# Performance work log

Measured on AMD Instinct MI355X. Metric: run time of the kernel, lower is better.

The kernel has to match this reference:

```python
import jax, jax.numpy as jnp
import numpy as np

N = 150_000      # nodes
E = 4_800_000    # edges (avg degree 32)
F_IN = 3
H = 16           # hidden_dim (module default)
DEPTH = 2        # -> DEPTH-1 = 1 mid layer


def setup_inputs() -> dict:
    key = jax.random.key(0)
    ks = jax.random.split(key, 6)
    x = jax.random.normal(ks[0], (N, F_IN), dtype=jnp.float32)
    edge_index = jax.random.randint(ks[1], (2, E), 0, N, dtype=jnp.int64)
    W_in = jax.random.normal(ks[2], (F_IN, H), dtype=jnp.float32) / np.sqrt(F_IN)
    b_in = jnp.zeros((H,), jnp.float32)
    W_mid = jax.random.normal(ks[3], (DEPTH - 1, H, H), dtype=jnp.float32) / np.sqrt(H)
    b_mid = jnp.zeros((DEPTH - 1, H), jnp.float32)
    W_out = jax.random.normal(ks[4], (H, 1), dtype=jnp.float32) / np.sqrt(H)
    b_out = jnp.zeros((1,), jnp.float32)
    return dict(x=x, edge_index=edge_index, W_in=W_in, b_in=b_in,
                W_mid=W_mid, b_mid=b_mid, W_out=W_out, b_out=b_out)


def _gcn(x, src, dst, norm, W, b):
    # GCNConv: X' = D^{-1/2}(A+I)D^{-1/2} X W + b  (self loops already in src/dst)
    h = x @ W                                   # [N, out]
    msg = h[src] * norm[:, None]                # gather + scale, [E+N, out]
    agg = jax.ops.segment_sum(msg, dst, num_segments=N)  # scatter-add
    return agg + b


def reference(x, edge_index, W_in, b_in, W_mid, b_mid, W_out, b_out):
    loops = jnp.arange(N, dtype=edge_index.dtype)
    src = jnp.concatenate([edge_index[0], loops])
    dst = jnp.concatenate([edge_index[1], loops])
    deg = jax.ops.segment_sum(jnp.ones_like(dst, x.dtype), dst, num_segments=N)
    dinv = jax.lax.rsqrt(jnp.where(deg > 0, deg, 1.0))  # deg >= 1 due to self loops
    norm = dinv[src] * dinv[dst]                # symmetric normalization per edge

    h = jax.nn.relu(_gcn(x, src, dst, norm, W_in, b_in))
    for i in range(DEPTH - 1):                  # dropout p=0.0 -> identity
        h = jax.nn.relu(_gcn(h, src, dst, norm, W_mid[i], b_mid[i]))
    out = _gcn(h, src, dst, norm, W_out, b_out)
    return jax.nn.sigmoid(out)                  # [N, 1]
```

## Files before the change

### kernel.cpp

```cpp
#include <hip/hip_runtime.h>
#include <math.h>

#define NN 150000
#define NE 4800000
#define HD 16
#define NBUCK 586
#define BSH 8
#define NBLK 256
#define CHUNK 18750
#define HCH 9375
#define NSCAN 150016
#define SCANB 147

__device__ __forceinline__ float bf2f(unsigned short u) {
    return __uint_as_float(((unsigned int)u) << 16);
}
__device__ __forceinline__ unsigned short f2bf(float f) {
    unsigned int x = __float_as_uint(f);
    return (unsigned short)((x + 0x7FFFu + ((x >> 16) & 1u)) >> 16);
}


__global__ __launch_bounds__(512) void k_part_count(const int* __restrict__ dst,
                                                    int* __restrict__ C) {
    __shared__ int h[NBUCK];
    for (int i = threadIdx.x; i < NBUCK; i += 512) h[i] = 0;
    __syncthreads();
    int base = blockIdx.x * CHUNK;
    for (int i = threadIdx.x; i < CHUNK; i += 512)
        atomicAdd(&h[dst[base + i] >> BSH], 1);
    __syncthreads();
    for (int i = threadIdx.x; i < NBUCK; i += 512) C[i * NBLK + blockIdx.x] = h[i];
}

__global__ void k_scanA(int* __restrict__ C, int* __restrict__ psum) {
    __shared__ int s[1024];
    int t = threadIdx.x;
    int i = blockIdx.x * 1024 + t;
    int v = (i < NSCAN) ? C[i] : 0;
    s[t] = v;
    __syncthreads();
    for (int off = 1; off < 1024; off <<= 1) {
        int x = (t >= off) ? s[t - off] : 0;
        __syncthreads();
        s[t] += x;
        __syncthreads();
    }
    if (i < NSCAN) C[i] = s[t] - v;
    if (t == 1023) psum[blockIdx.x] = s[1023];
}

__global__ void k_scanB(int* __restrict__ psum) {
    __shared__ int s[512];
    int t = threadIdx.x;
    int v = (t < SCANB) ? psum[t] : 0;
    s[t] = v;
    __syncthreads();
    for (int off = 1; off < 512; off <<= 1) {
        int x = (t >= off) ? s[t - off] : 0;
        __syncthreads();
        s[t] += x;
        __syncthreads();
    }
    if (t < SCANB) psum[t] = s[t] - v;
}

__global__ void k_scanC(int* __restrict__ C, const int* __restrict__ psum,
                        int* __restrict__ bstart) {
    int i = blockIdx.x * 1024 + threadIdx.x;
    if (i >= NSCAN) return;
    int v = C[i] + psum[blockIdx.x];
    C[i] = v;
    if ((i & (NBLK - 1)) == 0) bstart[i >> BSH] = v;
    if (i == 0) bstart[NBUCK] = NE;
}

__global__ __launch_bounds__(512) void k_part_scatter(const int* __restrict__ src,
                                                      const int* __restrict__ dst,
                                                      const int* __restrict__ C,
                                                      int* __restrict__ packed) {
    __shared__ int gcur[NBUCK];
    __shared__ int lcnt[NBUCK];
    __shared__ int lofs[NBUCK];
    __shared__ int stage[HCH];
    int tid = threadIdx.x;
    int bid = blockIdx.x;
    int m = ((bid & 7) << 5) | (bid >> 3);
    for (int i = tid; i < NBUCK; i += 512) gcur[i] = C[i * NBLK + m];
    for (int ph = 0; ph < 2; ++ph) {
        int base = m * CHUNK + ph * HCH;
        for (int i = tid; i < NBUCK; i += 512) lcnt[i] = 0;
        __syncthreads();
        for (int i = tid; i < HCH; i += 512)
            atomicAdd(&lcnt[dst[base + i] >> BSH], 1);
        __syncthreads();
        if (tid < 64) {
            int run = 0;
            for (int b0 = 0; b0 < NBUCK; b0 += 64) {
                int idx = b0 + tid;
                int c = (idx < NBUCK) ? lcnt[idx] : 0;
                int inc = c;
#pragma unroll
                for (int off = 1; off < 64; off <<= 1) {
                    int y = __shfl_up(inc, off);
                    if (tid >= off) inc += y;
                }
                if (idx < NBUCK) lofs[idx] = run + inc - c;
                run += __shfl(inc, 63);
            }
        }
        __syncthreads();
        for (int i = tid; i < HCH; i += 512) {
            int s = src[base + i];
            int d = dst[base + i];
            int b = d >> BSH;
            int pos = atomicAdd(&lofs[b], 1);
            stage[pos] = (s << BSH) | (d & 255);
        }
        __syncthreads();
        int wv = tid >> 6, ln = tid & 63;
        for (int b = wv; b < NBUCK; b += 8) {
            int c = lcnt[b];
            int ls = lofs[b] - c;
            int gs = gcur[b];
            for (int k = ln; k < c; k += 64) packed[gs + k] = stage[ls + k];
        }
        __syncthreads();
        for (int i = tid; i < NBUCK; i += 512) gcur[i] += lcnt[i];
    }
}

__global__ __launch_bounds__(256) void k_bucket_sort(const int* __restrict__ packed,
                                                     const int* __restrict__ bstart,
                                                     int* __restrict__ row_start,
                                                     float* __restrict__ dinv,
                                                     int* __restrict__ ssrc) {
    __shared__ int hist[256];
    __shared__ int fill[256];
    int b = blockIdx.x;
    int t = threadIdx.x;
    int v0 = b << BSH;
    int nv = min(256, NN - v0);
    int e0 = bstart[b], e1 = bstart[b + 1];
    hist[t] = 0;
    __syncthreads();
    for (int e = e0 + t; e < e1; e += 256)
        atomicAdd(&hist[packed[e] & 255], 1);
    __syncthreads();
    int cv = hist[t];
    __syncthreads();
    for (int off = 1; off < 256; off <<= 1) {
        int x = (t >= off) ? hist[t - off] : 0;
        __syncthreads();
        hist[t] += x;
        __syncthreads();
    }
    int excl = hist[t] - cv;
    if (t < nv) {
        row_start[v0 + t] = e0 + excl;
        fill[t] = e0 + excl;
        dinv[v0 + t] = rsqrtf((float)cv + 1.0f);
    }
    __syncthreads();
    for (int e = e0 + t; e < e1; e += 256) {
        int p = packed[e];
        int pos = atomicAdd(&fill[p & 255], 1);
        ssrc[pos] = p >> BSH;
    }
    if (b == 0 && t == 0) row_start[NN] = NE;
}

__global__ __launch_bounds__(256) void k_transform_in(const float* __restrict__ x,
                                                      const float* __restrict__ W,
                                                      const float* __restrict__ dinv,
                                                      unsigned short* __restrict__ t) {
    int gid = blockIdx.x * blockDim.x + threadIdx.x;
    if (gid >= NN * HD) return;
    int v = gid >> 4, j = gid & 15;
    float s = x[v * 3 + 0] * W[j] + x[v * 3 + 1] * W[HD + j] + x[v * 3 + 2] * W[2 * HD + j];
    t[gid] = f2bf(s * dinv[v]);
}

__global__ __launch_bounds__(512) void k_gather_mid(const int* __restrict__ row_start,
                                                    const int* __restrict__ ssrc,
                                                    const unsigned short* __restrict__ t,
                                                    const float* __restrict__ dinv,
                                                    const float* __restrict__ b,
                                                    const float* __restrict__ W,
                                                    unsigned short* __restrict__ tnext) {
    __shared__ float sW[HD * HD];
    __shared__ float sh[16 * HD];
    int tid = threadIdx.x;
    if (tid < HD * HD) sW[tid] = W[tid];
    int node = tid >> 5;
    int lane = tid & 31;
    int sub  = lane >> 3;
    int fl   = lane & 7;
    int v = blockIdx.x * 16 + node;
    int e0 = row_start[v], e1 = row_start[v + 1];
    float sx = 0.0f, sy = 0.0f;
    int e = e0 + sub;
    for (; e + 4 < e1; e += 8) {
        int sA = ssrc[e], sB = ssrc[e + 4];
        unsigned int wA = *(const unsigned int*)(t + (size_t)sA * HD + 2 * fl);
        unsigned int wB = *(const unsigned int*)(t + (size_t)sB * HD + 2 * fl);
        sx += bf2f((unsigned short)wA) + bf2f((unsigned short)wB);
        sy += bf2f((unsigned short)(wA >> 16)) + bf2f((unsigned short)(wB >> 16));
    }
    for (; e < e1; e += 4) {
        unsigned int w = *(const unsigned int*)(t + (size_t)ssrc[e] * HD + 2 * fl);
        sx += bf2f((unsigned short)w);
        sy += bf2f((unsigned short)(w >> 16));
    }
    if (sub == 0) {
        unsigned int w = *(const unsigned int*)(t + (size_t)v * HD + 2 * fl);
        sx += bf2f((unsigned short)w);
        sy += bf2f((unsigned short)(w >> 16));
    }
    sx += __shfl_xor(sx, 8);  sx += __shfl_xor(sx, 16);
    sy += __shfl_xor(sy, 8);  sy += __shfl_xor(sy, 16);
    if (sub == 0) {
        float di = dinv[v];
        sh[node * HD + 2 * fl]     = fmaxf(sx * di + b[2 * fl], 0.0f);
        sh[node * HD + 2 * fl + 1] = fmaxf(sy * di + b[2 * fl + 1], 0.0f);
    }
    __syncthreads();
    if (tid < 256) {
        int n = tid >> 4, jj = tid & 15;
        int vv = blockIdx.x * 16 + n;
        float o = 0.0f;
#pragma unroll
        for (int k = 0; k < HD; ++k) o += sh[n * HD + k] * sW[k * HD + jj];
        tnext[(size_t)vv * HD + jj] = f2bf(o * dinv[vv]);
    }
}

__global__ __launch_bounds__(512) void k_gather_out(const int* __restrict__ row_start,
                                                    const int* __restrict__ ssrc,
                                                    const unsigned short* __restrict__ t,
                                                    const float* __restrict__ dinv,
                                                    const float* __restrict__ b,
                                                    const float* __restrict__ Wout,
                                                    float* __restrict__ t3) {
    int tid = threadIdx.x;
    int node = tid >> 5;
    int lane = tid & 31;
    int sub  = lane >> 3;
    int fl   = lane & 7;
    int v = blockIdx.x * 16 + node;
    int e0 = row_start[v], e1 = row_start[v + 1];
    float sx = 0.0f, sy = 0.0f;
    int e = e0 + sub;
    for (; e + 4 < e1; e += 8) {
        int sA = ssrc[e], sB = ssrc[e + 4];
        unsigned int wA = *(const unsigned int*)(t + (size_t)sA * HD + 2 * fl);
        unsigned int wB = *(const unsigned int*)(t + (size_t)sB * HD + 2 * fl);
        sx += bf2f((unsigned short)wA) + bf2f((unsigned short)wB);
        sy += bf2f((unsigned short)(wA >> 16)) + bf2f((unsigned short)(wB >> 16));
    }
    for (; e < e1; e += 4) {
        unsigned int w = *(const unsigned int*)(t + (size_t)ssrc[e] * HD + 2 * fl);
        sx += bf2f((unsigned short)w);
        sy += bf2f((unsigned short)(w >> 16));
    }
    if (sub == 0) {
        unsigned int w = *(const unsigned int*)(t + (size_t)v * HD + 2 * fl);
        sx += bf2f((unsigned short)w);
        sy += bf2f((unsigned short)(w >> 16));
    }
    sx += __shfl_xor(sx, 8);  sx += __shfl_xor(sx, 16);
    sy += __shfl_xor(sy, 8);  sy += __shfl_xor(sy, 16);
    float di = dinv[v];
    float hx = fmaxf(sx * di + b[2 * fl], 0.0f);
    float hy = fmaxf(sy * di + b[2 * fl + 1], 0.0f);
    float d = hx * Wout[2 * fl] + hy * Wout[2 * fl + 1];
    d += __shfl_xor(d, 1);
    d += __shfl_xor(d, 2);
    d += __shfl_xor(d, 4);
    if (lane == 0) t3[v] = d * di;
}

__global__ __launch_bounds__(256) void k_gather_final(const int* __restrict__ row_start,
                                                      const int* __restrict__ ssrc,
                                                      const float* __restrict__ t3,
                                                      const float* __restrict__ dinv,
                                                      const float* __restrict__ b_out,
                                                      float* __restrict__ out) {
    int tid = threadIdx.x;
    int v = blockIdx.x * 16 + (tid >> 4);
    int l = tid & 15;
    int e0 = row_start[v], e1 = row_start[v + 1];
    float sum = 0.0f;
    for (int e = e0 + l; e < e1; e += 16) sum += t3[ssrc[e]];
    sum += __shfl_xor(sum, 1);
    sum += __shfl_xor(sum, 2);
    sum += __shfl_xor(sum, 4);
    sum += __shfl_xor(sum, 8);
    if (l == 0) {
        float z = (sum + t3[v]) * dinv[v] + b_out[0];
        out[v] = 1.0f / (1.0f + expf(-z));
    }
}

extern "C" void kernel_launch(void* const* d_in, const int* in_sizes, int n_in,
                              void* d_out, int out_size, void* d_ws, size_t ws_size,
                              hipStream_t stream) {
    const float* x     = (const float*)d_in[0];
    const int*   ei    = (const int*)d_in[1];
    const float* W_in  = (const float*)d_in[2];
    const float* b_in  = (const float*)d_in[3];
    const float* W_mid = (const float*)d_in[4];
    const float* b_mid = (const float*)d_in[5];
    const float* W_out = (const float*)d_in[6];
    const float* b_out = (const float*)d_in[7];
    float* out = (float*)d_out;

    const int* src = ei;
    const int* dst = ei + NE;

    char* p = (char*)d_ws;
    int*   C         = (int*)p;      p += sizeof(int) * NSCAN;
    int*   psum      = (int*)p;      p += sizeof(int) * 160;
    int*   bstart    = (int*)p;      p += sizeof(int) * (NBUCK + 2);
    int*   row_start = (int*)p;      p += sizeof(int) * (NN + 1);
    float* dinv      = (float*)p;    p += sizeof(float) * NN;
    int*   ssrc      = (int*)p;      p += sizeof(int) * (size_t)NE;
    int*   packed    = (int*)p;      p += sizeof(int) * (size_t)NE;
    unsigned short* tA = (unsigned short*)packed;
    unsigned short* tB = tA + (size_t)NN * HD;
    float* t3          = (float*)(tB + (size_t)NN * HD);

    const int gNH = (NN * HD + 255) / 256;
    const int gV  = NN / 16;

    k_part_count<<<NBLK, 512, 0, stream>>>(dst, C);
    k_scanA<<<SCANB, 1024, 0, stream>>>(C, psum);
    k_scanB<<<1, 512, 0, stream>>>(psum);
    k_scanC<<<SCANB, 1024, 0, stream>>>(C, psum, bstart);
    k_part_scatter<<<NBLK, 512, 0, stream>>>(src, dst, C, packed);
    k_bucket_sort<<<NBUCK, 256, 0, stream>>>(packed, bstart, row_start, dinv, ssrc);

    k_transform_in<<<gNH, 256, 0, stream>>>(x, W_in, dinv, tA);
    k_gather_mid<<<gV, 512, 0, stream>>>(row_start, ssrc, tA, dinv, b_in, W_mid, tB);
    k_gather_out<<<gV, 512, 0, stream>>>(row_start, ssrc, tB, dinv, b_mid, W_out, t3);
    k_gather_final<<<gV, 256, 0, stream>>>(row_start, ssrc, t3, dinv, b_out, out);
}
```

Before: 349.0 us.

## Split partition into 512 single-phase chunks and widen bucket sort blocks

The edge partition now uses 512 chunks of 9375 edges, one per block, in place of 256 chunks each handled in two sequential phases. Raw per-chunk counts are kept separately from the scanned offsets, so the scatter kernel reads its local counts directly instead of recounting. The copy-out now uses 16-lane groups per bucket. The bucket sort also moves from 256 to 512 threads per block. The goal is more parallelism and less serial work in the sort stage, at the cost of a scan that is twice as large.

Result: faster. 314.7 us (-9.8%).

```diff
diff --git a/kernel.cpp b/kernel.cpp
--- a/kernel.cpp
+++ b/kernel.cpp
@@ -6,11 +6,10 @@
 #define HD 16
 #define NBUCK 586
 #define BSH 8
-#define NBLK 256
-#define CHUNK 18750
+#define NCH 512
 #define HCH 9375
-#define NSCAN 150016
-#define SCANB 147
+#define NSCAN2 300032
+#define SCANB2 293
 
 __device__ __forceinline__ float bf2f(unsigned short u) {
     return __uint_as_float(((unsigned int)u) << 16);
@@ -22,22 +21,23 @@
 
 
 __global__ __launch_bounds__(512) void k_part_count(const int* __restrict__ dst,
-                                                    int* __restrict__ C) {
+                                                    int* __restrict__ Craw) {
     __shared__ int h[NBUCK];
     for (int i = threadIdx.x; i < NBUCK; i += 512) h[i] = 0;
     __syncthreads();
-    int base = blockIdx.x * CHUNK;
-    for (int i = threadIdx.x; i < CHUNK; i += 512)
+    int base = blockIdx.x * HCH;
+    for (int i = threadIdx.x; i < HCH; i += 512)
         atomicAdd(&h[dst[base + i] >> BSH], 1);
     __syncthreads();
-    for (int i = threadIdx.x; i < NBUCK; i += 512) C[i * NBLK + blockIdx.x] = h[i];
-}
-
-__global__ void k_scanA(int* __restrict__ C, int* __restrict__ psum) {
+    for (int i = threadIdx.x; i < NBUCK; i += 512) Craw[i * NCH + blockIdx.x] = h[i];
+}
+
+__global__ void k_scanA(const int* __restrict__ Craw, int* __restrict__ Cscan,
+                        int* __restrict__ psum) {
     __shared__ int s[1024];
     int t = threadIdx.x;
     int i = blockIdx.x * 1024 + t;
-    int v = (i < NSCAN) ? C[i] : 0;
+    int v = Craw[i];
     s[t] = v;
     __syncthreads();
     for (int off = 1; off < 1024; off <<= 1) {
@@ -46,14 +46,14 @@
         s[t] += x;
         __syncthreads();
     }
-    if (i < NSCAN) C[i] = s[t] - v;
+    Cscan[i] = s[t] - v;
     if (t == 1023) psum[blockIdx.x] = s[1023];
 }
 
 __global__ void k_scanB(int* __restrict__ psum) {
     __shared__ int s[512];
     int t = threadIdx.x;
-    int v = (t < SCANB) ? psum[t] : 0;
+    int v = (t < SCANB2) ? psum[t] : 0;
     s[t] = v;
     __syncthreads();
     for (int off = 1; off < 512; off <<= 1) {
@@ -62,75 +62,66 @@
         s[t] += x;
         __syncthreads();
     }
-    if (t < SCANB) psum[t] = s[t] - v;
-}
-
-__global__ void k_scanC(int* __restrict__ C, const int* __restrict__ psum,
+    if (t < SCANB2) psum[t] = s[t] - v;
+}
+
+__global__ void k_scanC(int* __restrict__ Cscan, const int* __restrict__ psum,
                         int* __restrict__ bstart) {
     int i = blockIdx.x * 1024 + threadIdx.x;
-    if (i >= NSCAN) return;
-    int v = C[i] + psum[blockIdx.x];
-    C[i] = v;
-    if ((i & (NBLK - 1)) == 0) bstart[i >> BSH] = v;
+    int v = Cscan[i] + psum[blockIdx.x];
+    Cscan[i] = v;
+    if ((i & (NCH - 1)) == 0) bstart[i >> 9] = v;
     if (i == 0) bstart[NBUCK] = NE;
 }
 
 __global__ __launch_bounds__(512) void k_part_scatter(const int* __restrict__ src,
                                                       const int* __restrict__ dst,
-                                                      const int* __restrict__ C,
+                                                      const int* __restrict__ Craw,
+                                                      const int* __restrict__ Cscan,
                                                       int* __restrict__ packed) {
-    __shared__ int gcur[NBUCK];
     __shared__ int lcnt[NBUCK];
     __shared__ int lofs[NBUCK];
     __shared__ int stage[HCH];
     int tid = threadIdx.x;
     int bid = blockIdx.x;
-    int m = ((bid & 7) << 5) | (bid >> 3);
-    for (int i = tid; i < NBUCK; i += 512) gcur[i] = C[i * NBLK + m];
-    for (int ph = 0; ph < 2; ++ph) {
-        int base = m * CHUNK + ph * HCH;
-        for (int i = tid; i < NBUCK; i += 512) lcnt[i] = 0;
-        __syncthreads();
-        for (int i = tid; i < HCH; i += 512)
-            atomicAdd(&lcnt[dst[base + i] >> BSH], 1);
-        __syncthreads();
-        if (tid < 64) {
-            int run = 0;
-            for (int b0 = 0; b0 < NBUCK; b0 += 64) {
-                int idx = b0 + tid;
-                int c = (idx < NBUCK) ? lcnt[idx] : 0;
-                int inc = c;
+    int m = ((bid & 7) << 6) | (bid >> 3);
+    for (int i = tid; i < NBUCK; i += 512) lcnt[i] = Craw[i * NCH + m];
+    __syncthreads();
+    if (tid < 64) {
+        int run = 0;
+        for (int b0 = 0; b0 < NBUCK; b0 += 64) {
+            int idx = b0 + tid;
+            int c = (idx < NBUCK) ? lcnt[idx] : 0;
+            int inc = c;
 #pragma unroll
-                for (int off = 1; off < 64; off <<= 1) {
-                    int y = __shfl_up(inc, off);
-                    if (tid >= off) inc += y;
-                }
-                if (idx < NBUCK) lofs[idx] = run + inc - c;
-                run += __shfl(inc, 63);
+            for (int off = 1; off < 64; off <<= 1) {
+                int y = __shfl_up(inc, off);
+                if (tid >= off) inc += y;
             }
+            if (idx < NBUCK) lofs[idx] = run + inc - c;
+            run += __shfl(inc, 63);
         }
-        __syncthreads();
-        for (int i = tid; i < HCH; i += 512) {
-            int s = src[base + i];
-            int d = dst[base + i];
-            int b = d >> BSH;
-            int pos = atomicAdd(&lofs[b], 1);
-            stage[pos] = (s << BSH) | (d & 255);
-        }
-        __syncthreads();
-        int wv = tid >> 6, ln = tid & 63;
-        for (int b = wv; b < NBUCK; b += 8) {
-            int c = lcnt[b];
-            int ls = lofs[b] - c;
-            int gs = gcur[b];
-            for (int k = ln; k < c; k += 64) packed[gs + k] = stage[ls + k];
-        }
-        __syncthreads();
-        for (int i = tid; i < NBUCK; i += 512) gcur[i] += lcnt[i];
-    }
-}
-
-__global__ __launch_bounds__(256) void k_bucket_sort(const int* __restrict__ packed,
+    }
+    __syncthreads();
+    int base = m * HCH;
+    for (int i = tid; i < HCH; i += 512) {
+        int s = src[base + i];
+        int d = dst[base + i];
+        int b = d >> BSH;
+        int pos = atomicAdd(&lofs[b], 1);
+        stage[pos] = (s << BSH) | (d & 255);
+    }
+    __syncthreads();
+    int grp = tid >> 4, ln = tid & 15;
+    for (int b = grp; b < NBUCK; b += 32) {
+        int c = lcnt[b];
+        int ls = lofs[b] - c;
+        int gs = Cscan[b * NCH + m];
+        for (int k = ln; k < c; k += 16) packed[gs + k] = stage[ls + k];
+    }
+}
+
+__global__ __launch_bounds__(512) void k_bucket_sort(const int* __restrict__ packed,
                                                      const int* __restrict__ bstart,
                                                      int* __restrict__ row_start,
                                                      float* __restrict__ dinv,
@@ -142,27 +133,27 @@
     int v0 = b << BSH;
     int nv = min(256, NN - v0);
     int e0 = bstart[b], e1 = bstart[b + 1];
-    hist[t] = 0;
-    __syncthreads();
-    for (int e = e0 + t; e < e1; e += 256)
+    if (t < 256) hist[t] = 0;
+    __syncthreads();
+    for (int e = e0 + t; e < e1; e += 512)
         atomicAdd(&hist[packed[e] & 255], 1);
     __syncthreads();
-    int cv = hist[t];
+    int cv = (t < 256) ? hist[t] : 0;
     __syncthreads();
     for (int off = 1; off < 256; off <<= 1) {
-        int x = (t >= off) ? hist[t - off] : 0;
-        __syncthreads();
-        hist[t] += x;
-        __syncthreads();
-    }
-    int excl = hist[t] - cv;
+        int x = (t >= off && t < 256) ? hist[t - off] : 0;
+        __syncthreads();
+        if (t < 256) hist[t] += x;
+        __syncthreads();
+    }
     if (t < nv) {
+        int excl = hist[t] - cv;
         row_start[v0 + t] = e0 + excl;
         fill[t] = e0 + excl;
         dinv[v0 + t] = rsqrtf((float)cv + 1.0f);
     }
     __syncthreads();
-    for (int e = e0 + t; e < e1; e += 256) {
+    for (int e = e0 + t; e < e1; e += 512) {
         int p = packed[e];
         int pos = atomicAdd(&fill[p & 255], 1);
         ssrc[pos] = p >> BSH;
@@ -319,8 +310,9 @@
     const int* dst = ei + NE;
 
     char* p = (char*)d_ws;
-    int*   C         = (int*)p;      p += sizeof(int) * NSCAN;
-    int*   psum      = (int*)p;      p += sizeof(int) * 160;
+    int*   Craw      = (int*)p;      p += sizeof(int) * NSCAN2;
+    int*   Cscan     = (int*)p;      p += sizeof(int) * NSCAN2;
+    int*   psum      = (int*)p;      p += sizeof(int) * 512;
     int*   bstart    = (int*)p;      p += sizeof(int) * (NBUCK + 2);
     int*   row_start = (int*)p;      p += sizeof(int) * (NN + 1);
     float* dinv      = (float*)p;    p += sizeof(float) * NN;
@@ -333,12 +325,12 @@
     const int gNH = (NN * HD + 255) / 256;
     const int gV  = NN / 16;
 
-    k_part_count<<<NBLK, 512, 0, stream>>>(dst, C);
-    k_scanA<<<SCANB, 1024, 0, stream>>>(C, psum);
+    k_part_count<<<NCH, 512, 0, stream>>>(dst, Craw);
+    k_scanA<<<SCANB2, 1024, 0, stream>>>(Craw, Cscan, psum);
     k_scanB<<<1, 512, 0, stream>>>(psum);
-    k_scanC<<<SCANB, 1024, 0, stream>>>(C, psum, bstart);
-    k_part_scatter<<<NBLK, 512, 0, stream>>>(src, dst, C, packed);
-    k_bucket_sort<<<NBUCK, 256, 0, stream>>>(packed, bstart, row_start, dinv, ssrc);
+    k_scanC<<<SCANB2, 1024, 0, stream>>>(Cscan, psum, bstart);
+    k_part_scatter<<<NCH, 512, 0, stream>>>(src, dst, Craw, Cscan, packed);
+    k_bucket_sort<<<NBUCK, 512, 0, stream>>>(packed, bstart, row_start, dinv, ssrc);
 
     k_transform_in<<<gNH, 256, 0, stream>>>(x, W_in, dinv, tA);
     k_gather_mid<<<gV, 512, 0, stream>>>(row_start, ssrc, tA, dinv, b_in, W_mid, tB);
```
